# Optimization experiments

Measured on AMD Instinct MI355X. Metric: run time of the kernel, lower is better.

## Reference

```python
import jax, jax.numpy as jnp
import numpy as np

N = 100_000      # nodes
E = 1_600_000    # edges
F_IN = 512       # input node features
H = 128          # hidden (num_hidden)
C = 64           # num_classes


def setup_inputs() -> dict:
    key = jax.random.key(0)
    ks = jax.random.split(key, 16)
    def lin(k, fi, fo):
        return (jax.random.normal(k, (fi, fo), jnp.float32) / np.sqrt(fi)).astype(jnp.float32)
    inp = {
        'x': jax.random.normal(ks[0], (N, F_IN), jnp.float32),
        'edge_index': jax.random.randint(ks[1], (2, E), 0, N, jnp.int32),
        'W0': lin(ks[2], F_IN, H), 'b0': jnp.zeros((H,), jnp.float32),
        'W1': lin(ks[3], H, H),    'b1': jnp.zeros((H,), jnp.float32),
        'W2': lin(ks[4], H, H),    'b2': jnp.zeros((H,), jnp.float32),
        'fc1_w': lin(ks[5], H, H), 'fc1_b': jnp.zeros((H,), jnp.float32),
        'fc2_w': lin(ks[6], H, H), 'fc2_b': jnp.zeros((H,), jnp.float32),
        'fc3_w': lin(ks[7], H, C), 'fc3_b': jnp.zeros((C,), jnp.float32),
    }
    return inp


def _gcn_norm(edge_index):
    # PyG GCNConv: add self-loops, symmetric normalization deg^-1/2 A deg^-1/2
    src = jnp.concatenate([edge_index[0], jnp.arange(N, dtype=edge_index.dtype)])
    dst = jnp.concatenate([edge_index[1], jnp.arange(N, dtype=edge_index.dtype)])
    deg = jax.ops.segment_sum(jnp.ones_like(dst, jnp.float32), dst, num_segments=N)
    dinv = jnp.where(deg > 0, jax.lax.rsqrt(deg), 0.0)
    norm = dinv[src] * dinv[dst]  # [E+N]
    return src, dst, norm


def _gcn_conv(x, W, b, src, dst, norm):
    h = x @ W + b                      # [N, H] transform first (fewer flops when F_in > H)
    msg = h[src] * norm[:, None]       # gather + scale, [E+N, H]
    return jax.ops.segment_sum(msg, dst, num_segments=N)  # scatter-add


def reference(x, edge_index, W0, b0, W1, b1, W2, b2,
              fc1_w, fc1_b, fc2_w, fc2_b, fc3_w, fc3_b):
    src, dst, norm = _gcn_norm(edge_index)
    y = jax.nn.relu(_gcn_conv(x, W0, b0, src, dst, norm))
    y = jax.nn.relu(_gcn_conv(y, W1, b1, src, dst, norm))
    y = jax.nn.relu(_gcn_conv(y, W2, b2, src, dst, norm))
    y = jax.nn.relu(y @ fc1_w + fc1_b)
    y = jax.nn.relu(y @ fc2_w + fc2_b)
    y = y @ fc3_w + fc3_b
    return jax.nn.log_softmax(y, axis=1)
```

## Files before the change

kernel.cpp:

```cpp
#include <hip/hip_runtime.h>
#include <hip/hip_bf16.h>
#include <cstdint>

typedef __hip_bfloat16 bf16;
typedef __hip_bfloat162 bf162;
typedef __bf16 bf16x8 __attribute__((ext_vector_type(8)));
typedef float f32x4 __attribute__((ext_vector_type(4)));

__global__ void detect_kernel(const unsigned short* __restrict__ xr, int* __restrict__ flag) {
  if (threadIdx.x == 0 && blockIdx.x == 0) {
    int pass = 0;
    for (int i = 0; i < 64; ++i) {
      unsigned short h = xr[2 * i];
      int e = (h >> 7) & 0xFF;
      if (e >= 110 && e <= 140) pass++;
    }
    *flag = (pass >= 32) ? 1 : 0;
  }
}

struct CvtDesc {
  const void* src;
  void* dst;
  int n, fi, fo, mode;
};
struct CvtAll { CvtDesc d[12]; };

__global__ void convert_all_kernel(CvtAll all, const int* __restrict__ flag) {
  CvtDesc dd = all.d[blockIdx.y];
  int isbf = *flag;
  for (int i = blockIdx.x * blockDim.x + threadIdx.x; i < dd.n; i += gridDim.x * blockDim.x) {
    float v = isbf ? __bfloat162float(((const bf16*)dd.src)[i]) : ((const float*)dd.src)[i];
    if (dd.mode) {
      int k = i / dd.fo, nn = i - k * dd.fo;
      ((__bf16*)dd.dst)[(size_t)nn * dd.fi + k] = (__bf16)v;
    } else {
      ((float*)dd.dst)[i] = v;
    }
  }
}


__global__ void count_kernel(const int* __restrict__ dst, int* __restrict__ deg, int E) {
  int i = blockIdx.x * blockDim.x + threadIdx.x;
  if (i < E) atomicAdd(&deg[dst[i]], 1);
}

__global__ void scan_block_kernel(const int* __restrict__ counts, int* __restrict__ excl,
                                  int* __restrict__ bsum, float* __restrict__ dinv, int n) {
  __shared__ int sd[1024];
  int t = threadIdx.x;
  int i = blockIdx.x * 1024 + t;
  int v = (i < n) ? counts[i] : 0;
  if (i < n) dinv[i] = rsqrtf((float)(v + 1));
  sd[t] = v;
  __syncthreads();
  for (int off = 1; off < 1024; off <<= 1) {
    int x = (t >= off) ? sd[t - off] : 0;
    __syncthreads();
    sd[t] += x;
    __syncthreads();
  }
  if (i < n) excl[i] = sd[t] - v;
  if (t == 1023) bsum[blockIdx.x] = sd[1023];
}

__global__ void scan_sums_kernel(int* __restrict__ bsum, int nb, int* __restrict__ row_ptr, int n) {
  __shared__ int sd[1024];
  int t = threadIdx.x;
  int v = (t < nb) ? bsum[t] : 0;
  sd[t] = v;
  __syncthreads();
  for (int off = 1; off < 1024; off <<= 1) {
    int x = (t >= off) ? sd[t - off] : 0;
    __syncthreads();
    sd[t] += x;
    __syncthreads();
  }
  if (t < nb) bsum[t] = sd[t] - v;
  if (t == 1023) row_ptr[n] = sd[1023];
}

__global__ void scan_add_kernel(int* __restrict__ excl, const int* __restrict__ bsum, int n) {
  int i = blockIdx.x * blockDim.x + threadIdx.x;
  if (i < n) excl[i] += bsum[i >> 10];
}

__global__ void fill_kernel(const int* __restrict__ src, const int* __restrict__ dst,
                            const int* __restrict__ row_ptr, int* __restrict__ deg,
                            int* __restrict__ col, int E) {
  int i = blockIdx.x * blockDim.x + threadIdx.x;
  if (i < E) {
    int d = dst[i];
    int k = atomicSub(&deg[d], 1) - 1;
    col[row_ptr[d] + k] = src[i];
  }
}

__device__ __forceinline__ void gload_lds16(const void* g, void* l) {
  __builtin_amdgcn_global_load_lds(
      (const __attribute__((address_space(1))) void*)g,
      (__attribute__((address_space(3))) void*)l, 16, 0, 0);
}


template <int K, int ADUAL>
__global__ __launch_bounds__(256) void gemm_mfma_kernel(
    const void* __restrict__ Ain, const __bf16* __restrict__ Bt,
    const float* __restrict__ bias, bf16* __restrict__ C,
    int M, const float* __restrict__ rowscale, int do_relu,
    const int* __restrict__ flag) {
  constexpr int BK = 64;
  constexpr int NT = K / BK;
  __shared__ __align__(16) __bf16 As[2][128 * BK];
  __shared__ __align__(16) __bf16 Bs[2][128 * BK];

  const int abf = ADUAL ? flag[0] : 1;
  int t = threadIdx.x;
  int wave = t >> 6, lane = t & 63;
  int l15 = lane & 15, quad = lane >> 4;
  int wm = wave >> 1, wn = wave & 1;
  int rowbase = blockIdx.x * 128;
  const __bf16* Ab = (const __bf16*)Ain;
  const float* Af = (const float*)Ain;

  int srow = t >> 3;
  int sslot = t & 7;
  int xslot = sslot ^ (srow & 7);

  int sArow[4];
#pragma unroll
  for (int i = 0; i < 4; ++i) {
    int r = rowbase + i * 32 + srow;
    sArow[i] = (r < M) ? r : (M - 1);
  }

  f32x4 acc[4][4];
#pragma unroll
  for (int mt = 0; mt < 4; ++mt)
#pragma unroll
    for (int nt = 0; nt < 4; ++nt) acc[mt][nt] = (f32x4){0.f, 0.f, 0.f, 0.f};

  auto stage = [&](int kt, int buf) {
    int kbase = kt * BK + xslot * 8;
    if (abf) {
#pragma unroll
      for (int i = 0; i < 4; ++i)
        gload_lds16(Ab + (size_t)sArow[i] * K + kbase, &As[buf][t * 8 + i * 2048]);
    } else {
#pragma unroll
      for (int i = 0; i < 4; ++i) {
        const float* p = Af + (size_t)sArow[i] * K + kbase;
        bf16x8 v;
#pragma unroll
        for (int j = 0; j < 8; ++j) v[j] = (__bf16)p[j];
        *(bf16x8*)&As[buf][t * 8 + i * 2048] = v;
      }
    }
#pragma unroll
    for (int i = 0; i < 4; ++i)
      gload_lds16(Bt + (size_t)(i * 32 + srow) * K + kbase, &Bs[buf][t * 8 + i * 2048]);
  };

  auto compute = [&](int buf) {
#pragma unroll
    for (int c = 0; c < 2; ++c) {
      bf16x8 av[4], bv[4];
#pragma unroll
      for (int mt = 0; mt < 4; ++mt) {
        int row = wm * 64 + mt * 16 + l15;
        int slot = (c * 4 + quad) ^ (row & 7);
        av[mt] = *(const bf16x8*)&As[buf][row * BK + slot * 8];
      }
#pragma unroll
      for (int nt = 0; nt < 4; ++nt) {
        int row = wn * 64 + nt * 16 + l15;
        int slot = (c * 4 + quad) ^ (row & 7);
        bv[nt] = *(const bf16x8*)&Bs[buf][row * BK + slot * 8];
      }
#pragma unroll
      for (int mt = 0; mt < 4; ++mt)
#pragma unroll
        for (int nt = 0; nt < 4; ++nt)
          acc[mt][nt] =
              __builtin_amdgcn_mfma_f32_16x16x32_bf16(av[mt], bv[nt], acc[mt][nt], 0, 0, 0);
    }
  };

  stage(0, 0);
  if (abf) {
#pragma unroll
    for (int kt = 0; kt < NT; ++kt) {
      int cur = kt & 1;
      if (kt + 1 < NT) {
        stage(kt + 1, cur ^ 1);
        asm volatile("s_waitcnt vmcnt(8)" ::: "memory");
      } else {
        asm volatile("s_waitcnt vmcnt(0)" ::: "memory");
      }
      __builtin_amdgcn_sched_barrier(0);
      __builtin_amdgcn_s_barrier();
      __builtin_amdgcn_sched_barrier(0);
      compute(cur);
      __builtin_amdgcn_sched_barrier(0);
      __builtin_amdgcn_s_barrier();
    }
  } else {
    __syncthreads();
#pragma unroll
    for (int kt = 0; kt < NT; ++kt) {
      int cur = kt & 1;
      if (kt + 1 < NT) stage(kt + 1, cur ^ 1);
      compute(cur);
      __syncthreads();
    }
  }

#pragma unroll
  for (int mt = 0; mt < 4; ++mt) {
    int r0 = rowbase + wm * 64 + mt * 16 + quad * 4;
#pragma unroll
    for (int nt = 0; nt < 4; ++nt) {
      int c = wn * 64 + nt * 16 + l15;
      float bs = bias[c];
#pragma unroll
      for (int i = 0; i < 4; ++i) {
        int r = r0 + i;
        if (r < M) {
          float v = acc[mt][nt][i] + bs;
          if (rowscale) v *= rowscale[r];
          if (do_relu) v = fmaxf(v, 0.f);
          C[(size_t)r * 128 + c] = __float2bfloat16(v);
        }
      }
    }
  }
}


__global__ __launch_bounds__(256) void gather_kernel(
    const bf16* __restrict__ g, const int* __restrict__ row_ptr, const int* __restrict__ col,
    const float* __restrict__ dinv, bf16* __restrict__ y, int n) {
  int wave = threadIdx.x >> 6;
  int lane = threadIdx.x & 63;
  int node = blockIdx.x * 4 + wave;
  if (node >= n) return;
  const bf162* gp = (const bf162*)g;
  bf162 sv = gp[(size_t)node * 64 + lane];
  float ax = __bfloat162float(sv.x), ay = __bfloat162float(sv.y);
  float bx = 0.f, by = 0.f;
  int beg = row_ptr[node], end = row_ptr[node + 1];

  if (beg < end) {
    int sc[8], sn[8];
    float mc[8], mn[8];
#pragma unroll
    for (int j = 0; j < 8; ++j) {
      int ee = beg + j;
      bool ok = ee < end;
      sc[j] = col[ok ? ee : beg];
      mc[j] = ok ? 1.f : 0.f;
    }
    for (int e = beg; e < end; e += 8) {
      bf162 v[8];
#pragma unroll
      for (int j = 0; j < 8; ++j) v[j] = gp[(size_t)sc[j] * 64 + lane];
      int e2 = e + 8;
      bool more = e2 < end;
      if (more) {
#pragma unroll
        for (int j = 0; j < 8; ++j) {
          int ee = e2 + j;
          bool ok = ee < end;
          sn[j] = col[ok ? ee : beg];
          mn[j] = ok ? 1.f : 0.f;
        }
      }
#pragma unroll
      for (int j = 0; j < 8; j += 2) {
        ax = fmaf(mc[j], __bfloat162float(v[j].x), ax);
        ay = fmaf(mc[j], __bfloat162float(v[j].y), ay);
        bx = fmaf(mc[j + 1], __bfloat162float(v[j + 1].x), bx);
        by = fmaf(mc[j + 1], __bfloat162float(v[j + 1].y), by);
      }
      if (more) {
#pragma unroll
        for (int j = 0; j < 8; ++j) {
          sc[j] = sn[j];
          mc[j] = mn[j];
        }
      }
    }
  }
  float dv = dinv[node];
  float ox = fmaxf((ax + bx) * dv, 0.f);
  float oy = fmaxf((ay + by) * dv, 0.f);
  bf162 o;
  o.x = __float2bfloat16(ox);
  o.y = __float2bfloat16(oy);
  ((bf162*)y)[(size_t)node * 64 + lane] = o;
}


__global__ __launch_bounds__(256) void fc_chain_kernel(
    const bf16* __restrict__ yin, const __bf16* __restrict__ W1t,
    const float* __restrict__ b1, const __bf16* __restrict__ W2t,
    const float* __restrict__ b2, const __bf16* __restrict__ W3t,
    const float* __restrict__ b3, void* __restrict__ out, int M,
    const int* __restrict__ flag) {
  constexpr int LDH = 136;
  __shared__ __align__(16) __bf16 h1[128 * LDH];
  __shared__ __align__(16) __bf16 h2[128 * LDH];
  const int isbf = flag[0];
  int t = threadIdx.x;
  int wave = t >> 6, lane = t & 63;
  int l15 = lane & 15, quad = lane >> 4;
  int wm = wave >> 1, wn = wave & 1;
  int rowbase = blockIdx.x * 128;

  f32x4 acc[4][4];
  bf16x8 aA[4], bA[4], aB[4], bB[4];

  auto zacc = [&]() {
#pragma unroll
    for (int mt = 0; mt < 4; ++mt)
#pragma unroll
      for (int nt = 0; nt < 4; ++nt) acc[mt][nt] = (f32x4){0.f, 0.f, 0.f, 0.f};
  };
  auto mfma16 = [&](const bf16x8 (&av)[4], const bf16x8 (&bv)[4]) {
#pragma unroll
    for (int mt = 0; mt < 4; ++mt)
#pragma unroll
      for (int nt = 0; nt < 4; ++nt)
        acc[mt][nt] =
            __builtin_amdgcn_mfma_f32_16x16x32_bf16(av[mt], bv[nt], acc[mt][nt], 0, 0, 0);
  };

  int arow[4];
#pragma unroll
  for (int mt = 0; mt < 4; ++mt) {
    int r = rowbase + wm * 64 + mt * 16 + l15;
    arow[mt] = (r < M) ? r : (M - 1);
  }
  auto ld1 = [&](int kc, bf16x8 (&av)[4], bf16x8 (&bv)[4]) {
    int ko = kc + quad * 8;
#pragma unroll
    for (int mt = 0; mt < 4; ++mt)
      av[mt] = *(const bf16x8*)(yin + (size_t)arow[mt] * 128 + ko);
#pragma unroll
    for (int nt = 0; nt < 4; ++nt)
      bv[nt] = *(const bf16x8*)(W1t + (size_t)(wn * 64 + nt * 16 + l15) * 128 + ko);
  };
  zacc();
  ld1(0, aA, bA);
  ld1(32, aB, bB);
  mfma16(aA, bA);
  ld1(64, aA, bA);
  mfma16(aB, bB);
  ld1(96, aB, bB);
  mfma16(aA, bA);
  mfma16(aB, bB);
#pragma unroll
  for (int mt = 0; mt < 4; ++mt) {
    int rl0 = wm * 64 + mt * 16 + quad * 4;
#pragma unroll
    for (int nt = 0; nt < 4; ++nt) {
      int c = wn * 64 + nt * 16 + l15;
      float bs = b1[c];
#pragma unroll
      for (int i = 0; i < 4; ++i)
        h1[(rl0 + i) * LDH + c] = (__bf16)fmaxf(acc[mt][nt][i] + bs, 0.f);
    }
  }
  __syncthreads();

  auto ld2 = [&](int kc, bf16x8 (&av)[4], bf16x8 (&bv)[4]) {
    int ko = kc + quad * 8;
#pragma unroll
    for (int mt = 0; mt < 4; ++mt)
      av[mt] = *(const bf16x8*)&h1[(wm * 64 + mt * 16 + l15) * LDH + ko];
#pragma unroll
    for (int nt = 0; nt < 4; ++nt)
      bv[nt] = *(const bf16x8*)(W2t + (size_t)(wn * 64 + nt * 16 + l15) * 128 + ko);
  };
  zacc();
  ld2(0, aA, bA);
  ld2(32, aB, bB);
  mfma16(aA, bA);
  ld2(64, aA, bA);
  mfma16(aB, bB);
  ld2(96, aB, bB);
  mfma16(aA, bA);
  mfma16(aB, bB);
#pragma unroll
  for (int mt = 0; mt < 4; ++mt) {
    int rl0 = wm * 64 + mt * 16 + quad * 4;
#pragma unroll
    for (int nt = 0; nt < 4; ++nt) {
      int c = wn * 64 + nt * 16 + l15;
      float bs = b2[c];
#pragma unroll
      for (int i = 0; i < 4; ++i)
        h2[(rl0 + i) * LDH + c] = (__bf16)fmaxf(acc[mt][nt][i] + bs, 0.f);
    }
  }
  __syncthreads();

  f32x4 acc3[2][4];
#pragma unroll
  for (int mt = 0; mt < 2; ++mt)
#pragma unroll
    for (int nt = 0; nt < 4; ++nt) acc3[mt][nt] = (f32x4){0.f, 0.f, 0.f, 0.f};
  bf16x8 a3A[2], a3B[2];
  auto ld3 = [&](int kc, bf16x8 (&av)[2], bf16x8 (&bv)[4]) {
    int ko = kc + quad * 8;
#pragma unroll
    for (int mt = 0; mt < 2; ++mt)
      av[mt] = *(const bf16x8*)&h2[(wave * 32 + mt * 16 + l15) * LDH + ko];
#pragma unroll
    for (int nt = 0; nt < 4; ++nt)
      bv[nt] = *(const bf16x8*)(W3t + (size_t)(nt * 16 + l15) * 128 + ko);
  };
  auto mfma8 = [&](const bf16x8 (&av)[2], const bf16x8 (&bv)[4]) {
#pragma unroll
    for (int mt = 0; mt < 2; ++mt)
#pragma unroll
      for (int nt = 0; nt < 4; ++nt)
        acc3[mt][nt] =
            __builtin_amdgcn_mfma_f32_16x16x32_bf16(av[mt], bv[nt], acc3[mt][nt], 0, 0, 0);
  };
  ld3(0, a3A, bA);
  ld3(32, a3B, bB);
  mfma8(a3A, bA);
  ld3(64, a3A, bA);
  mfma8(a3B, bB);
  ld3(96, a3B, bB);
  mfma8(a3A, bA);
  mfma8(a3B, bB);

  float bcol[4];
#pragma unroll
  for (int nt = 0; nt < 4; ++nt) bcol[nt] = b3[nt * 16 + l15];

#pragma unroll
  for (int mt = 0; mt < 2; ++mt) {
#pragma unroll
    for (int i = 0; i < 4; ++i) {
      int r = rowbase + wave * 32 + mt * 16 + quad * 4 + i;
      float v0 = acc3[mt][0][i] + bcol[0];
      float v1 = acc3[mt][1][i] + bcol[1];
      float v2 = acc3[mt][2][i] + bcol[2];
      float v3 = acc3[mt][3][i] + bcol[3];
      float m = fmaxf(fmaxf(v0, v1), fmaxf(v2, v3));
#pragma unroll
      for (int off = 8; off > 0; off >>= 1) m = fmaxf(m, __shfl_xor(m, off, 16));
      float s = __expf(v0 - m) + __expf(v1 - m) + __expf(v2 - m) + __expf(v3 - m);
#pragma unroll
      for (int off = 8; off > 0; off >>= 1) s += __shfl_xor(s, off, 16);
      float ls = m + __logf(s);
      if (r < M) {
        if (isbf) {
          bf16* op = (bf16*)out + (size_t)r * 64 + l15;
          op[0] = __float2bfloat16(v0 - ls);
          op[16] = __float2bfloat16(v1 - ls);
          op[32] = __float2bfloat16(v2 - ls);
          op[48] = __float2bfloat16(v3 - ls);
        } else {
          float* op = (float*)out + (size_t)r * 64 + l15;
          op[0] = v0 - ls;
          op[16] = v1 - ls;
          op[32] = v2 - ls;
          op[48] = v3 - ls;
        }
      }
    }
  }
}


extern "C" void kernel_launch(void* const* d_in, const int* in_sizes, int n_in,
                              void* d_out, int out_size, void* d_ws, size_t ws_size,
                              hipStream_t stream) {
  const void* x = d_in[0];
  const int* ei = (const int*)d_in[1];

  const int N = in_sizes[0] / 512;
  const int E = in_sizes[1] / 2;
  const int* srcp = ei;
  const int* dstp = ei + E;

  char* ws = (char*)d_ws;
  size_t off = 0;
  auto alloc = [&](size_t bytes) {
    void* p = ws + off;
    off = (off + bytes + 255) & ~(size_t)255;
    return p;
  };
  int*    flag    = (int*)alloc(4);
  int*    deg     = (int*)alloc((size_t)N * 4);
  int*    row_ptr = (int*)alloc((size_t)(N + 1) * 4);
  int*    col     = (int*)alloc((size_t)E * 4);
  float*  dinv    = (float*)alloc((size_t)N * 4);
  int*    bsum    = (int*)alloc(1024 * 4);
  __bf16* W0t     = (__bf16*)alloc((size_t)512 * 128 * 2);
  __bf16* W1t     = (__bf16*)alloc((size_t)128 * 128 * 2);
  __bf16* W2t     = (__bf16*)alloc((size_t)128 * 128 * 2);
  __bf16* fc1t    = (__bf16*)alloc((size_t)128 * 128 * 2);
  __bf16* fc2t    = (__bf16*)alloc((size_t)128 * 128 * 2);
  __bf16* fc3t    = (__bf16*)alloc((size_t)64 * 128 * 2);
  float*  b0f     = (float*)alloc(128 * 4);
  float*  b1f     = (float*)alloc(128 * 4);
  float*  b2f     = (float*)alloc(128 * 4);
  float*  fc1bf   = (float*)alloc(128 * 4);
  float*  fc2bf   = (float*)alloc(128 * 4);
  float*  fc3bf   = (float*)alloc(64 * 4);
  bf16*   gbuf    = (bf16*)alloc((size_t)N * 128 * 2);
  bf16*   ybuf    = (bf16*)alloc((size_t)N * 128 * 2);

  const int tb = 256;

  detect_kernel<<<1, 64, 0, stream>>>((const unsigned short*)x, flag);

  CvtAll ca;
  ca.d[0]  = {d_in[2],  W0t,   512 * 128, 512, 128, 1};
  ca.d[1]  = {d_in[4],  W1t,   128 * 128, 128, 128, 1};
  ca.d[2]  = {d_in[6],  W2t,   128 * 128, 128, 128, 1};
  ca.d[3]  = {d_in[8],  fc1t,  128 * 128, 128, 128, 1};
  ca.d[4]  = {d_in[10], fc2t,  128 * 128, 128, 128, 1};
  ca.d[5]  = {d_in[3],  b0f,   128, 0, 0, 0};
  ca.d[6]  = {d_in[5],  b1f,   128, 0, 0, 0};
  ca.d[7]  = {d_in[7],  b2f,   128, 0, 0, 0};
  ca.d[8]  = {d_in[9],  fc1bf, 128, 0, 0, 0};
  ca.d[9]  = {d_in[11], fc2bf, 128, 0, 0, 0};
  ca.d[10] = {d_in[12], fc3t,  128 * 64, 128, 64, 1};
  ca.d[11] = {d_in[13], fc3bf, 64, 0, 0, 0};
  convert_all_kernel<<<dim3(64, 12), 256, 0, stream>>>(ca, flag);

  hipMemsetAsync(deg, 0, (size_t)N * 4, stream);

  count_kernel<<<(E + tb - 1) / tb, tb, 0, stream>>>(dstp, deg, E);
  int nb = (N + 1023) / 1024;
  scan_block_kernel<<<nb, 1024, 0, stream>>>(deg, row_ptr, bsum, dinv, N);
  scan_sums_kernel<<<1, 1024, 0, stream>>>(bsum, nb, row_ptr, N);
  scan_add_kernel<<<(N + tb - 1) / tb, tb, 0, stream>>>(row_ptr, bsum, N);
  fill_kernel<<<(E + tb - 1) / tb, tb, 0, stream>>>(srcp, dstp, row_ptr, deg, col, E);

  int gemm_blocks = (N + 127) / 128;
  int gat_blocks = (N + 3) / 4;

  gemm_mfma_kernel<512, 1><<<gemm_blocks, 256, 0, stream>>>(x, W0t, b0f, gbuf, N, dinv, 0, flag);
  gather_kernel<<<gat_blocks, 256, 0, stream>>>(gbuf, row_ptr, col, dinv, ybuf, N);
  gemm_mfma_kernel<128, 0><<<gemm_blocks, 256, 0, stream>>>(ybuf, W1t, b1f, gbuf, N, dinv, 0, flag);
  gather_kernel<<<gat_blocks, 256, 0, stream>>>(gbuf, row_ptr, col, dinv, ybuf, N);
  gemm_mfma_kernel<128, 0><<<gemm_blocks, 256, 0, stream>>>(ybuf, W2t, b2f, gbuf, N, dinv, 0, flag);
  gather_kernel<<<gat_blocks, 256, 0, stream>>>(gbuf, row_ptr, col, dinv, ybuf, N);
  fc_chain_kernel<<<gemm_blocks, 256, 0, stream>>>(ybuf, fc1t, fc1bf, fc2t, fc2bf,
                                                   fc3t, fc3bf, d_out, N, flag);
}
```

Baseline: 808.3 us.

## Add persistent contiguous-panel GEMM for the first 512-wide layer

Replaces the first-layer K=512 GEMM with a persistent kernel of 256 blocks. Each block loads full 64-row by 512-column A panels with contiguous row reads into swizzled LDS, double-buffered through registers so the next panel's global load overlaps the current MFMA work. The B operand is read straight from global memory or cache instead of LDS. This aims to improve streaming bandwidth on the large x read (fp32 or bf16) and cut per-K-tile synchronisation. In exchange it uses 128KB of LDS per block, which limits occupancy to one block per CU, and it relies on cache hits for the repeated B loads.

```diff
diff --git a/kernel.cpp b/kernel.cpp
--- a/kernel.cpp
+++ b/kernel.cpp
@@ -101,6 +101,145 @@
   __builtin_amdgcn_global_load_lds(
       (const __attribute__((address_space(1))) void*)g,
       (__attribute__((address_space(3))) void*)l, 16, 0, 0);
+}
+
+
+template <int ADUAL>
+__global__ __launch_bounds__(256) void gemm512_contig_kernel(
+    const void* __restrict__ Ain, const __bf16* __restrict__ Bt,
+    const float* __restrict__ bias, bf16* __restrict__ C,
+    int M, const float* __restrict__ rowscale, int do_relu,
+    const int* __restrict__ flag) {
+  __shared__ __align__(16) __bf16 Ap[2][64 * 512];
+  const int abf = ADUAL ? flag[0] : 1;
+  int t = threadIdx.x;
+  int wave = t >> 6, lane = t & 63;
+  int l15 = lane & 15, quad = lane >> 4;
+  int wm = wave >> 1, wn = wave & 1;
+  const __bf16* Ab = (const __bf16*)Ain;
+  const float* Af = (const float*)Ain;
+  const int G = gridDim.x;
+  const int npan = (M + 63) >> 6;
+
+  bf16x8 v[16];
+
+  auto ldpanel = [&](int p) {
+#pragma unroll
+    for (int j = 0; j < 16; ++j) {
+      int gr = p * 64 + j * 4 + wave;
+      if (gr >= M) gr = M - 1;
+      if (abf) {
+        v[j] = *(const bf16x8*)(Ab + (size_t)gr * 512 + lane * 8);
+      } else {
+        const float* pr = Af + (size_t)gr * 512 + lane * 8;
+        f32x4 a = *(const f32x4*)pr;
+        f32x4 b = *(const f32x4*)(pr + 4);
+#pragma unroll
+        for (int k = 0; k < 4; ++k) {
+          v[j][k] = (__bf16)a[k];
+          v[j][4 + k] = (__bf16)b[k];
+        }
+      }
+    }
+  };
+
+  auto wrpanel = [&](int buf) {
+#pragma unroll
+    for (int j = 0; j < 16; ++j) {
+      int r = j * 4 + wave;
+      int byte = (r << 10) + lane * 16;
+      byte ^= (r & 7) << 4;
+      *(bf16x8*)((char*)&Ap[buf][0] + byte) = v[j];
+    }
+  };
+
+  int p = blockIdx.x;
+  if (p >= npan) return;
+
+  ldpanel(p);
+  wrpanel(0);
+  __syncthreads();
+  int buf = 0;
+
+  while (true) {
+    int pn = p + G;
+    bool more = pn < npan;
+    if (more) ldpanel(pn);
+
+    f32x4 acc[2][4];
+#pragma unroll
+    for (int mt = 0; mt < 2; ++mt)
+#pragma unroll
+      for (int nt = 0; nt < 4; ++nt) acc[mt][nt] = (f32x4){0.f, 0.f, 0.f, 0.f};
+
+    bf16x8 avA[2], avB[2], bA[4], bB[4];
+    auto ldA = [&](int c, bf16x8 (&av)[2]) {
+#pragma unroll
+      for (int mt = 0; mt < 2; ++mt) {
+        int row = wm * 32 + mt * 16 + l15;
+        int byte = (row << 10) + c * 64 + quad * 16;
+        byte ^= (row & 7) << 4;
+        av[mt] = *(const bf16x8*)((const char*)&Ap[buf][0] + byte);
+      }
+    };
+    auto ldB = [&](int c, bf16x8 (&bv)[4]) {
+      int ko = c * 32 + quad * 8;
+#pragma unroll
+      for (int nt = 0; nt < 4; ++nt)
+        bv[nt] = *(const bf16x8*)(Bt + (size_t)(wn * 64 + nt * 16 + l15) * 512 + ko);
+    };
+    auto mm = [&](const bf16x8 (&av)[2], const bf16x8 (&bv)[4]) {
+#pragma unroll
+      for (int mt = 0; mt < 2; ++mt)
+#pragma unroll
+        for (int nt = 0; nt < 4; ++nt)
+          acc[mt][nt] =
+              __builtin_amdgcn_mfma_f32_16x16x32_bf16(av[mt], bv[nt], acc[mt][nt], 0, 0, 0);
+    };
+
+    ldA(0, avA);
+    ldB(0, bA);
+#pragma unroll
+    for (int c = 0; c < 16; c += 2) {
+      if (c + 1 < 16) {
+        ldA(c + 1, avB);
+        ldB(c + 1, bB);
+      }
+      mm(avA, bA);
+      if (c + 2 < 16) {
+        ldA(c + 2, avA);
+        ldB(c + 2, bA);
+      }
+      if (c + 1 < 16) mm(avB, bB);
+    }
+
+#pragma unroll
+    for (int mt = 0; mt < 2; ++mt) {
+      int r0 = p * 64 + wm * 32 + mt * 16 + quad * 4;
+#pragma unroll
+      for (int nt = 0; nt < 4; ++nt) {
+        int c = wn * 64 + nt * 16 + l15;
+        float bs = bias[c];
+#pragma unroll
+        for (int i = 0; i < 4; ++i) {
+          int r = r0 + i;
+          if (r < M) {
+            float val = acc[mt][nt][i] + bs;
+            if (rowscale) val *= rowscale[r];
+            if (do_relu) val = fmaxf(val, 0.f);
+            C[(size_t)r * 128 + c] = __float2bfloat16(val);
+          }
+        }
+      }
+    }
+
+    if (!more) break;
+    __syncthreads();
+    wrpanel(buf ^ 1);
+    __syncthreads();
+    buf ^= 1;
+    p = pn;
+  }
 }
 
 
@@ -548,7 +687,7 @@
   int gemm_blocks = (N + 127) / 128;
   int gat_blocks = (N + 3) / 4;
 
-  gemm_mfma_kernel<512, 1><<<gemm_blocks, 256, 0, stream>>>(x, W0t, b0f, gbuf, N, dinv, 0, flag);
+  gemm512_contig_kernel<1><<<256, 256, 0, stream>>>(x, W0t, b0f, gbuf, N, dinv, 0, flag);
   gather_kernel<<<gat_blocks, 256, 0, stream>>>(gbuf, row_ptr, col, dinv, ybuf, N);
   gemm_mfma_kernel<128, 0><<<gemm_blocks, 256, 0, stream>>>(ybuf, W1t, b1f, gbuf, N, dinv, 0, flag);
   gather_kernel<<<gat_blocks, 256, 0, stream>>>(gbuf, row_ptr, col, dinv, ybuf, N);
```

Result: slower. 846.9 us (+4.8%).

## Fuse CSR fill into first GEMM launch via interleaved block roles

Applied to the files above, without the earlier changes.

The standalone CSR column-fill kernel is removed, and its work moves into the first layer's GEMM launch. The grid is doubled: odd blocks run a grid-strided atomic fill of col, even blocks do the 512-wide GEMM tile. This overlaps the memory-and-atomic-bound fill with the compute-bound GEMM and saves one launch. In exchange, fill blocks hold the same large static LDS allocation, which may limit occupancy, and the GEMM body is duplicated.

```diff
diff --git a/kernel.cpp b/kernel.cpp
--- a/kernel.cpp
+++ b/kernel.cpp
@@ -86,21 +86,158 @@
   if (i < n) excl[i] += bsum[i >> 10];
 }
 
-__global__ void fill_kernel(const int* __restrict__ src, const int* __restrict__ dst,
-                            const int* __restrict__ row_ptr, int* __restrict__ deg,
-                            int* __restrict__ col, int E) {
-  int i = blockIdx.x * blockDim.x + threadIdx.x;
-  if (i < E) {
-    int d = dst[i];
-    int k = atomicSub(&deg[d], 1) - 1;
-    col[row_ptr[d] + k] = src[i];
-  }
-}
-
 __device__ __forceinline__ void gload_lds16(const void* g, void* l) {
   __builtin_amdgcn_global_load_lds(
       (const __attribute__((address_space(1))) void*)g,
       (__attribute__((address_space(3))) void*)l, 16, 0, 0);
+}
+
+
+template <int K, int ADUAL>
+__global__ __launch_bounds__(256) void gemm_fill_kernel(
+    const void* __restrict__ Ain, const __bf16* __restrict__ Bt,
+    const float* __restrict__ bias, bf16* __restrict__ C,
+    int M, const float* __restrict__ rowscale, int do_relu,
+    const int* __restrict__ flag,
+    const int* __restrict__ srcp, const int* __restrict__ dstp,
+    const int* __restrict__ row_ptr, int* __restrict__ deg,
+    int* __restrict__ col, int E) {
+  constexpr int BK = 64;
+  constexpr int NT = K / BK;
+  __shared__ __align__(16) __bf16 As[2][128 * BK];
+  __shared__ __align__(16) __bf16 Bs[2][128 * BK];
+
+  int bid = blockIdx.x >> 1;
+  if (blockIdx.x & 1) {
+    int nfb = gridDim.x >> 1;
+    for (int i = bid * 256 + (int)threadIdx.x; i < E; i += nfb * 256) {
+      int d = dstp[i];
+      int k = atomicSub(&deg[d], 1) - 1;
+      col[row_ptr[d] + k] = srcp[i];
+    }
+    return;
+  }
+
+  const int abf = ADUAL ? flag[0] : 1;
+  int t = threadIdx.x;
+  int wave = t >> 6, lane = t & 63;
+  int l15 = lane & 15, quad = lane >> 4;
+  int wm = wave >> 1, wn = wave & 1;
+  int rowbase = bid * 128;
+  const __bf16* Ab = (const __bf16*)Ain;
+  const float* Af = (const float*)Ain;
+
+  int srow = t >> 3;
+  int sslot = t & 7;
+  int xslot = sslot ^ (srow & 7);
+
+  int sArow[4];
+#pragma unroll
+  for (int i = 0; i < 4; ++i) {
+    int r = rowbase + i * 32 + srow;
+    sArow[i] = (r < M) ? r : (M - 1);
+  }
+
+  f32x4 acc[4][4];
+#pragma unroll
+  for (int mt = 0; mt < 4; ++mt)
+#pragma unroll
+    for (int nt = 0; nt < 4; ++nt) acc[mt][nt] = (f32x4){0.f, 0.f, 0.f, 0.f};
+
+  auto stage = [&](int kt, int buf) {
+    int kbase = kt * BK + xslot * 8;
+    if (abf) {
+#pragma unroll
+      for (int i = 0; i < 4; ++i)
+        gload_lds16(Ab + (size_t)sArow[i] * K + kbase, &As[buf][t * 8 + i * 2048]);
+    } else {
+#pragma unroll
+      for (int i = 0; i < 4; ++i) {
+        const float* p = Af + (size_t)sArow[i] * K + kbase;
+        bf16x8 v;
+#pragma unroll
+        for (int j = 0; j < 8; ++j) v[j] = (__bf16)p[j];
+        *(bf16x8*)&As[buf][t * 8 + i * 2048] = v;
+      }
+    }
+#pragma unroll
+    for (int i = 0; i < 4; ++i)
+      gload_lds16(Bt + (size_t)(i * 32 + srow) * K + kbase, &Bs[buf][t * 8 + i * 2048]);
+  };
+
+  auto compute = [&](int buf) {
+#pragma unroll
+    for (int c = 0; c < 2; ++c) {
+      bf16x8 av[4], bv[4];
+#pragma unroll
+      for (int mt = 0; mt < 4; ++mt) {
+        int row = wm * 64 + mt * 16 + l15;
+        int slot = (c * 4 + quad) ^ (row & 7);
+        av[mt] = *(const bf16x8*)&As[buf][row * BK + slot * 8];
+      }
+#pragma unroll
+      for (int nt = 0; nt < 4; ++nt) {
+        int row = wn * 64 + nt * 16 + l15;
+        int slot = (c * 4 + quad) ^ (row & 7);
+        bv[nt] = *(const bf16x8*)&Bs[buf][row * BK + slot * 8];
+      }
+#pragma unroll
+      for (int mt = 0; mt < 4; ++mt)
+#pragma unroll
+        for (int nt = 0; nt < 4; ++nt)
+          acc[mt][nt] =
+              __builtin_amdgcn_mfma_f32_16x16x32_bf16(av[mt], bv[nt], acc[mt][nt], 0, 0, 0);
+    }
+  };
+
+  stage(0, 0);
+  if (abf) {
+#pragma unroll
+    for (int kt = 0; kt < NT; ++kt) {
+      int cur = kt & 1;
+      if (kt + 1 < NT) {
+        stage(kt + 1, cur ^ 1);
+        asm volatile("s_waitcnt vmcnt(8)" ::: "memory");
+      } else {
+        asm volatile("s_waitcnt vmcnt(0)" ::: "memory");
+      }
+      __builtin_amdgcn_sched_barrier(0);
+      __builtin_amdgcn_s_barrier();
+      __builtin_amdgcn_sched_barrier(0);
+      compute(cur);
+      __builtin_amdgcn_sched_barrier(0);
+      __builtin_amdgcn_s_barrier();
+    }
+  } else {
+    __syncthreads();
+#pragma unroll
+    for (int kt = 0; kt < NT; ++kt) {
+      int cur = kt & 1;
+      if (kt + 1 < NT) stage(kt + 1, cur ^ 1);
+      compute(cur);
+      __syncthreads();
+    }
+  }
+
+#pragma unroll
+  for (int mt = 0; mt < 4; ++mt) {
+    int r0 = rowbase + wm * 64 + mt * 16 + quad * 4;
+#pragma unroll
+    for (int nt = 0; nt < 4; ++nt) {
+      int c = wn * 64 + nt * 16 + l15;
+      float bs = bias[c];
+#pragma unroll
+      for (int i = 0; i < 4; ++i) {
+        int r = r0 + i;
+        if (r < M) {
+          float v = acc[mt][nt][i] + bs;
+          if (rowscale) v *= rowscale[r];
+          if (do_relu) v = fmaxf(v, 0.f);
+          C[(size_t)r * 128 + c] = __float2bfloat16(v);
+        }
+      }
+    }
+  }
 }
 
 
@@ -543,12 +680,12 @@
   scan_block_kernel<<<nb, 1024, 0, stream>>>(deg, row_ptr, bsum, dinv, N);
   scan_sums_kernel<<<1, 1024, 0, stream>>>(bsum, nb, row_ptr, N);
   scan_add_kernel<<<(N + tb - 1) / tb, tb, 0, stream>>>(row_ptr, bsum, N);
-  fill_kernel<<<(E + tb - 1) / tb, tb, 0, stream>>>(srcp, dstp, row_ptr, deg, col, E);
 
   int gemm_blocks = (N + 127) / 128;
   int gat_blocks = (N + 3) / 4;
 
-  gemm_mfma_kernel<512, 1><<<gemm_blocks, 256, 0, stream>>>(x, W0t, b0f, gbuf, N, dinv, 0, flag);
+  gemm_fill_kernel<512, 1><<<2 * gemm_blocks, 256, 0, stream>>>(
+      x, W0t, b0f, gbuf, N, dinv, 0, flag, srcp, dstp, row_ptr, deg, col, E);
   gather_kernel<<<gat_blocks, 256, 0, stream>>>(gbuf, row_ptr, col, dinv, ybuf, N);
   gemm_mfma_kernel<128, 0><<<gemm_blocks, 256, 0, stream>>>(ybuf, W1t, b1f, gbuf, N, dinv, 0, flag);
   gather_kernel<<<gat_blocks, 256, 0, stream>>>(gbuf, row_ptr, col, dinv, ybuf, N);
```

Result: faster. 778.9 us (-3.6%).
